# Kernel optimization log

Hardware: AMD Instinct MI355X
Metric: run time of the kernel (lower is better)

The kernel has to match this reference:

```python
import jax, jax.numpy as jnp
from jax import lax
import numpy as np

B, L, D, H, OMEGA = 8, 1024, 2048, 512, 5


def _conv1d(x_ncw, W_oiw, b):
    # x: [B, C_in, L], W: [C_out, C_in, K] -> [B, C_out, L-K+1]
    y = lax.conv_general_dilated(x_ncw, W_oiw, window_strides=(1,),
                                 padding='VALID',
                                 dimension_numbers=('NCH', 'OIH', 'NCH'))
    return y + b[None, :, None]


def _lstm_dir(xs, Wih, Whh, bih, bhh, reverse):
    # xs: [B, T, I] -> hs: [B, T, H] (PyTorch gate order i,f,g,o)
    nB, T, _ = xs.shape
    nH = Whh.shape[1]
    xs_t = jnp.swapaxes(xs, 0, 1)  # [T, B, I]
    bias = bih + bhh

    def step(carry, xt):
        h, c = carry
        g = xt @ Wih.T + h @ Whh.T + bias
        i, f, gg, o = jnp.split(g, 4, axis=-1)
        c = jax.nn.sigmoid(f) * c + jax.nn.sigmoid(i) * jnp.tanh(gg)
        h = jax.nn.sigmoid(o) * jnp.tanh(c)
        return (h, c), h

    init = (jnp.zeros((nB, nH), xs.dtype), jnp.zeros((nB, nH), xs.dtype))
    _, hs = lax.scan(step, init, xs_t, reverse=reverse)
    return jnp.swapaxes(hs, 0, 1)


def setup_inputs() -> dict:
    key = jax.random.key(0)
    ks = jax.random.split(key, 16)
    s = 0.02
    inp = {
        'x': jax.random.normal(ks[0], (B, L, D), jnp.float32),
        'Wdb': jax.random.normal(ks[1], (H, D, OMEGA), jnp.float32) * s,
        'bdb': jnp.zeros((H,), jnp.float32),
        'Wda': jax.random.normal(ks[2], (H, D, OMEGA), jnp.float32) * s,
        'bda': jnp.zeros((H,), jnp.float32),
        'Wr': jax.random.normal(ks[3], (H, D, 2 * OMEGA), jnp.float32) * s,
        'br': jnp.zeros((H,), jnp.float32),
        'Wih_fw': jax.random.normal(ks[4], (4 * H, H + 1), jnp.float32) * s,
        'Whh_fw': jax.random.normal(ks[5], (4 * H, H), jnp.float32) * s,
        'bih_fw': jnp.zeros((4 * H,), jnp.float32),
        'bhh_fw': jnp.zeros((4 * H,), jnp.float32),
        'Wih_bw': jax.random.normal(ks[6], (4 * H, H + 1), jnp.float32) * s,
        'Whh_bw': jax.random.normal(ks[7], (4 * H, H), jnp.float32) * s,
        'bih_bw': jnp.zeros((4 * H,), jnp.float32),
        'bhh_bw': jnp.zeros((4 * H,), jnp.float32),
        'Wfc': jax.random.normal(ks[8], (1, 2 * H), jnp.float32) * s,
        'bfc': jnp.zeros((1,), jnp.float32),
    }
    return inp


def reference(x, Wdb, bdb, Wda, bda, Wr, br,
              Wih_fw, Whh_fw, bih_fw, bhh_fw,
              Wih_bw, Whh_bw, bih_bw, bhh_bw, Wfc, bfc):
    T = L - 2 * OMEGA  # number of center positions
    x_c = jnp.swapaxes(x, 1, 2)  # [B, D, L]
    # Each per-window conv with kernel==window length is one output of a full
    # VALID conv; batch all centers via three full convs + offset slicing.
    db = _conv1d(x_c, Wdb, bdb)  # [B, H, L-OMEGA+1]; index t == window [t, t+OMEGA)
    da = _conv1d(x_c, Wda, bda)
    r = _conv1d(x_c, Wr, br)     # [B, H, L-2*OMEGA+1]
    # center c in [OMEGA, L-OMEGA): before window starts at c-OMEGA, after at c
    vts_d = jnp.sum(db[:, :, :T] * da[:, :, OMEGA:OMEGA + T], axis=1)  # [B, T]
    vts_r = jnp.swapaxes(r[:, :, :T], 1, 2)  # [B, T, H] (maxpool over len-1 = identity)
    joint = jnp.concatenate([vts_r, vts_d[..., None]], axis=-1)  # [B, T, H+1]
    h_fw = _lstm_dir(joint, Wih_fw, Whh_fw, bih_fw, bhh_fw, reverse=False)
    h_bw = _lstm_dir(joint, Wih_bw, Whh_bw, bih_bw, bhh_bw, reverse=True)
    lstm_out = jnp.concatenate([h_fw, h_bw], axis=-1)  # [B, T, 2H]
    logits = (lstm_out @ Wfc.T + bfc)[..., 0]  # [B, T]
    return jax.nn.sigmoid(logits)
```

## Files before the change

kernel.cpp:

```cpp
#include <hip/hip_runtime.h>

#define BB 8
#define LL 1024
#define DD 2048
#define HHH 512
#define OM 5
#define T_STEPS 1014
#define MROWS (BB * T_STEPS)
#define SENT 0xFFFFFFFFu

typedef __bf16 bf16;
typedef bf16 bf16x8 __attribute__((ext_vector_type(8)));
typedef bf16 bf16x4 __attribute__((ext_vector_type(4)));
typedef float f32x4 __attribute__((ext_vector_type(4)));
typedef unsigned int u32;
typedef unsigned long long u64;
typedef u64 u64x2 __attribute__((ext_vector_type(2)));

__device__ __forceinline__ float sigm(float x) { return 1.0f / (1.0f + __expf(-x)); }
__device__ __forceinline__ float tanh_f(float x) { return 2.0f / (1.0f + __expf(-2.0f * x)) - 1.0f; }
__device__ __forceinline__ u32 bfbits(float x) {
    bf16 b = (bf16)x;
    unsigned short s = __builtin_bit_cast(unsigned short, b);
    return (u32)s;
}
__device__ __forceinline__ float bits2f(u32 v) {
    unsigned short s = (unsigned short)(v & 0xffffu);
    return (float)__builtin_bit_cast(bf16, s);
}
__device__ __forceinline__ u64 al64(const u64* p) {
    return __hip_atomic_load(p, __ATOMIC_RELAXED, __HIP_MEMORY_SCOPE_AGENT);
}
__device__ __forceinline__ bf16x8 quad2frag(u64 lo, u64 hi) {
    u64x2 t; t[0] = lo; t[1] = hi;
    return __builtin_bit_cast(bf16x8, t);
}
__device__ __forceinline__ bool quad_ok(u64 lo, u64 hi) {
    return ((u32)lo != SENT) & ((u32)(lo >> 32) != SENT) &
           ((u32)hi != SENT) & ((u32)(hi >> 32) != SENT);
}

#if defined(__has_builtin)
#if __has_builtin(__builtin_amdgcn_global_load_lds)
#define HAS_GLL 1
#endif
#endif
#ifndef HAS_GLL
#define HAS_GLL 0
#endif

#if HAS_GLL
__device__ __forceinline__ void llds16(const bf16* g, bf16* l) {
    __builtin_amdgcn_global_load_lds((const __attribute__((address_space(1))) void*)g,
                                     (__attribute__((address_space(3))) void*)l, 16, 0, 0);
}
#endif


__global__ void cast_x_kernel(const float* __restrict__ x, bf16* __restrict__ xb, int n4) {
    int i = blockIdx.x * 256 + threadIdx.x;
    if (i >= n4) return;
    float4 v = ((const float4*)x)[i];
    bf16x4 w = { (bf16)v.x, (bf16)v.y, (bf16)v.z, (bf16)v.w };
    *(bf16x4*)(xb + (long)i * 4) = w;
}

__global__ void prep_convw(const float* __restrict__ Wdb, const float* __restrict__ Wda,
                           const float* __restrict__ Wr,
                           bf16* __restrict__ Bdb, bf16* __restrict__ Bda, bf16* __restrict__ Br) {
    int idx = blockIdx.x * 256 + threadIdx.x;
    if (idx >= HHH * DD) return;
    int h = idx >> 11, d = idx & 2047;
#pragma unroll
    for (int s = 0; s < 5; ++s) {
        Bdb[(long)h * 10240 + s * DD + d] = (bf16)Wdb[(long)(h * DD + d) * 5 + s];
        Bda[(long)h * 10240 + s * DD + d] = (bf16)Wda[(long)(h * DD + d) * 5 + s];
    }
#pragma unroll
    for (int s = 0; s < 10; ++s) {
        Br[(long)h * 20480 + s * DD + d] = (bf16)Wr[(long)(h * DD + d) * 10 + s];
    }
}

__global__ void prep_wihc(const float* __restrict__ Wih_fw, const float* __restrict__ bih_fw,
                          const float* __restrict__ bhh_fw,
                          const float* __restrict__ Wih_bw, const float* __restrict__ bih_bw,
                          const float* __restrict__ bhh_bw, bf16* __restrict__ Wihc) {
    int c = blockIdx.x;
    int tid = threadIdx.x;
    int dir = c >> 11;
    int jg = c & 2047;
    int j = jg >> 2, g = jg & 3;
    int row = g * 512 + j;
    const float* Wih = dir ? Wih_bw : Wih_fw;
    bf16* o = Wihc + (long)c * 544;
    for (int k = tid; k < 512; k += 256) o[k] = (bf16)Wih[(long)row * 513 + k];
    if (tid == 0) {
        float bias = dir ? (bih_bw[row] + bhh_bw[row]) : (bih_fw[row] + bhh_fw[row]);
        float w512 = Wih[(long)row * 513 + 512];
        bf16 hw = (bf16)w512;
        float lw = w512 - (float)hw;
        o[512] = hw; o[513] = hw; o[514] = (bf16)lw; o[515] = (bf16)bias;
    }
    if (tid >= 4 && tid < 32) o[512 + tid] = (bf16)0.0f;
}

__global__ void init_kernel(u32* __restrict__ hf, u32* __restrict__ hb) {
    const long n4 = (long)(T_STEPS + 1) * 1024;
    long i = (long)blockIdx.x * 256 + threadIdx.x;
    if (i >= 2 * n4) return;
    u32* base = (i < n4) ? hf : hb;
    long k = (i < n4) ? i : (i - n4);
    u32 v = (k < 1024) ? 0u : SENT;
    uint4 val; val.x = v; val.y = v; val.z = v; val.w = v;
    ((uint4*)base)[k] = val;
}

__global__ __launch_bounds__(256, 2)
void gemm_bt(const bf16* __restrict__ A, const bf16* __restrict__ Bm, void* __restrict__ Cout,
             const float* __restrict__ cbias, int M, int K, int windowed, int shift,
             int lda, int ldc, int cmode) {
    __shared__ bf16 Ash[128 * 32];
    __shared__ bf16 Bsh[128 * 32];
    const int tid = threadIdx.x;
    const int m0 = blockIdx.x * 128;
    const int n0 = blockIdx.y * 128;

    long aoff[2], boff[2];
#pragma unroll
    for (int it = 0; it < 2; ++it) {
        int idx = it * 256 + tid;
        int r = idx & 127, koct = idx >> 7;
        int mg = m0 + r; if (mg >= M) mg = M - 1;
        long abase;
        if (windowed) {
            int b = mg / T_STEPS;
            int t = mg - b * T_STEPS;
            abase = ((long)(b * LL + t + shift)) * DD;
        } else {
            abase = (long)mg * lda;
        }
        aoff[it] = abase + koct * 8;
        boff[it] = (long)(n0 + r) * K + koct * 8;
    }

    const int wave = tid >> 6, lane = tid & 63;
    const int wr = (wave >> 1) * 64;
    const int wc = (wave & 1) * 64;
    const int q = lane >> 4, mm = lane & 15;

    f32x4 acc[4][4] = {};

    for (int k0 = 0; k0 < K; k0 += 32) {
#if HAS_GLL
        __syncthreads();
#pragma unroll
        for (int it = 0; it < 2; ++it) {
            bf16* la = Ash + (size_t)(it * 256 + wave * 64) * 8;
            bf16* lb = Bsh + (size_t)(it * 256 + wave * 64) * 8;
            llds16(A + aoff[it] + k0, la);
            llds16(Bm + boff[it] + k0, lb);
        }
        __syncthreads();
#else
        uint4 av[2], bv[2];
#pragma unroll
        for (int it = 0; it < 2; ++it) {
            av[it] = *(const uint4*)(A + aoff[it] + k0);
            bv[it] = *(const uint4*)(Bm + boff[it] + k0);
        }
        __syncthreads();
#pragma unroll
        for (int it = 0; it < 2; ++it) {
            int idx = it * 256 + tid;
            *(uint4*)((char*)Ash + idx * 16) = av[it];
            *(uint4*)((char*)Bsh + idx * 16) = bv[it];
        }
        __syncthreads();
#endif
        bf16x8 af[4], bfr[4];
#pragma unroll
        for (int i = 0; i < 4; ++i) {
            af[i]  = *(const bf16x8*)((char*)Ash + q * 2048 + (wr + i * 16 + mm) * 16);
            bfr[i] = *(const bf16x8*)((char*)Bsh + q * 2048 + (wc + i * 16 + mm) * 16);
        }
#pragma unroll
        for (int i = 0; i < 4; ++i)
#pragma unroll
            for (int j = 0; j < 4; ++j)
                acc[i][j] = __builtin_amdgcn_mfma_f32_16x16x32_bf16(af[i], bfr[j], acc[i][j], 0, 0, 0);
    }

#pragma unroll
    for (int i = 0; i < 4; ++i) {
        int rowb = m0 + wr + i * 16 + q * 4;
#pragma unroll
        for (int j = 0; j < 4; ++j) {
            int col = n0 + wc + j * 16 + mm;
            float bias = cbias ? cbias[col] : 0.0f;
#pragma unroll
            for (int r = 0; r < 4; ++r) {
                int gr = rowb + r;
                if (gr < M) {
                    float v = acc[i][j][r] + bias;
                    if (cmode == 0) ((float*)Cout)[(long)gr * ldc + col] = v;
                    else            ((bf16*)Cout)[(long)gr * ldc + col] = (bf16)v;
                }
            }
        }
    }
}

__global__ void vts_kernel(const float* __restrict__ dbuf, const float* __restrict__ dabuf,
                           bf16* __restrict__ joint) {
    int gid = blockIdx.x * blockDim.x + threadIdx.x;
    int wid = gid >> 6, lane = gid & 63;
    if (wid >= MROWS) return;
    const float* p1 = dbuf + (long)wid * 512 + lane * 8;
    const float* p2 = dabuf + (long)wid * 512 + lane * 8;
    float s = 0.0f;
#pragma unroll
    for (int j = 0; j < 8; ++j) s += p1[j] * p2[j];
#pragma unroll
    for (int off = 32; off > 0; off >>= 1) s += __shfl_down(s, off);
    bf16* row = joint + (long)wid * 544;
    if (lane == 0) {
        bf16 hv = (bf16)s;
        float lo = s - (float)hv;
        row[512] = hv; row[513] = (bf16)lo; row[514] = hv; row[515] = (bf16)1.0f;
    }
    if (lane >= 4 && lane < 32) row[512 + lane] = (bf16)0.0f;
}

__global__ __launch_bounds__(64) __attribute__((amdgpu_waves_per_eu(1, 1)))
void lstm_kernel(const float* __restrict__ Whh_fw, const float* __restrict__ Whh_bw,
                 const float* __restrict__ gih, u32* __restrict__ hist_fw,
                 u32* __restrict__ hist_bw) {
    const int wgid = blockIdx.x;
    const int dir = wgid >> 6;
    const int w = wgid & 63;
    const int j0 = w * 8;
    const int lane = threadIdx.x;
    const float* Whh = dir ? Whh_bw : Whh_fw;
    u32* hist = dir ? hist_bw : hist_fw;

    const int q = lane >> 4, mm = lane & 15;

    bf16x8 afrag[2][16];
#pragma unroll
    for (int mt = 0; mt < 2; ++mt) {
        int rl = mt * 16 + mm;
        int u = rl >> 2, g = rl & 3;
        const float* wrow = Whh + ((long)(g * 512 + j0 + u)) * 512;
#pragma unroll
        for (int ks = 0; ks < 16; ++ks) {
            int base = ks * 32 + q * 8;
            bf16x8 f;
#pragma unroll
            for (int j = 0; j < 8; ++j) {
                int col = base + (j >> 1) + ((j & 1) << 2);
                f[j] = (bf16)wrow[col];
            }
            afrag[mt][ks] = f;
        }
    }

    float c0 = 0.0f, c1 = 0.0f;
    const bool valid = (mm < 8);
    const int bcl = valid ? mm : 0;

    int tcur = dir ? (T_STEPS - 1) : 0;
    const float* gp0 = gih + ((long)(bcl * T_STEPS + tcur)) * 4096 + dir * 2048 + (j0 + q) * 4;
    f32x4 pg0 = *(const f32x4*)gp0;
    f32x4 pg1 = *(const f32x4*)(gp0 + 16);

    for (int s = 0; s < T_STEPS; ++s) {
        const u64* hrow = (const u64*)(hist + (long)s * 4096 + mm * 256);
        u64 wa[16], wb[16];
#pragma unroll
        for (int i = 0; i < 16; ++i) { wa[i] = 0ull; wb[i] = 0ull; }

        u32 pa = valid ? 0xFFu : 0u;
        if (valid) {
#pragma unroll
            for (int ks = 0; ks < 8; ++ks) {
                const u64* p = hrow + ks * 8 + q * 2;
                wa[2 * ks]     = al64(p + 0);
                wa[2 * ks + 1] = al64(p + 1);
            }
        }
        for (;;) {
#pragma unroll
            for (int ks = 0; ks < 8; ++ks) {
                if (pa & (1u << ks)) {
                    if (quad_ok(wa[2 * ks], wa[2 * ks + 1])) pa &= ~(1u << ks);
                }
            }
            if (__all((int)(pa == 0u))) break;
            __builtin_amdgcn_s_sleep(1);
#pragma unroll
            for (int ks = 0; ks < 8; ++ks) {
                if (pa & (1u << ks)) {
                    const u64* p = hrow + ks * 8 + q * 2;
                    wa[2 * ks]     = al64(p + 0);
                    wa[2 * ks + 1] = al64(p + 1);
                }
            }
        }

        u32 pb = valid ? 0xFFu : 0u;
        if (valid) {
#pragma unroll
            for (int ks = 0; ks < 8; ++ks) {
                const u64* p = hrow + (ks + 8) * 8 + q * 2;
                wb[2 * ks]     = al64(p + 0);
                wb[2 * ks + 1] = al64(p + 1);
            }
        }

        f32x4 acc0 = pg0, acc1 = pg1;
        f32x4 acc0b = {0.0f, 0.0f, 0.0f, 0.0f}, acc1b = {0.0f, 0.0f, 0.0f, 0.0f};

        if (s + 1 < T_STEPS) {
            int tn = dir ? (T_STEPS - 2 - s) : (s + 1);
            const float* gpn = gih + ((long)(bcl * T_STEPS + tn)) * 4096 + dir * 2048 + (j0 + q) * 4;
            pg0 = *(const f32x4*)gpn;
            pg1 = *(const f32x4*)(gpn + 16);
        }

#pragma unroll
        for (int ks = 0; ks < 8; ++ks) {
            bf16x8 b = quad2frag(wa[2 * ks], wa[2 * ks + 1]);
            acc0 = __builtin_amdgcn_mfma_f32_16x16x32_bf16(afrag[0][ks], b, acc0, 0, 0, 0);
            acc1 = __builtin_amdgcn_mfma_f32_16x16x32_bf16(afrag[1][ks], b, acc1, 0, 0, 0);
        }

        for (;;) {
#pragma unroll
            for (int ks = 0; ks < 8; ++ks) {
                if (pb & (1u << ks)) {
                    if (quad_ok(wb[2 * ks], wb[2 * ks + 1])) pb &= ~(1u << ks);
                }
            }
            if (__all((int)(pb == 0u))) break;
            __builtin_amdgcn_s_sleep(1);
#pragma unroll
            for (int ks = 0; ks < 8; ++ks) {
                if (pb & (1u << ks)) {
                    const u64* p = hrow + (ks + 8) * 8 + q * 2;
                    wb[2 * ks]     = al64(p + 0);
                    wb[2 * ks + 1] = al64(p + 1);
                }
            }
        }

#pragma unroll
        for (int ks = 0; ks < 8; ++ks) {
            bf16x8 b = quad2frag(wb[2 * ks], wb[2 * ks + 1]);
            acc0b = __builtin_amdgcn_mfma_f32_16x16x32_bf16(afrag[0][ks + 8], b, acc0b, 0, 0, 0);
            acc1b = __builtin_amdgcn_mfma_f32_16x16x32_bf16(afrag[1][ks + 8], b, acc1b, 0, 0, 0);
        }
        acc0 += acc0b;
        acc1 += acc1b;

        float ig = sigm(acc0[0]), fg = sigm(acc0[1]), gg = tanh_f(acc0[2]), og = sigm(acc0[3]);
        c0 = fg * c0 + ig * gg;
        float h0 = og * tanh_f(c0);
        ig = sigm(acc1[0]); fg = sigm(acc1[1]); gg = tanh_f(acc1[2]); og = sigm(acc1[3]);
        c1 = fg * c1 + ig * gg;
        float h1 = og * tanh_f(c1);

        if (valid) {
            u32 pw = bfbits(h0) | (bfbits(h1) << 16);
            __hip_atomic_store(hist + (long)(s + 1) * 4096 + mm * 256 + (j0 >> 1) + q, pw,
                               __ATOMIC_RELAXED, __HIP_MEMORY_SCOPE_AGENT);
        }
    }
}

__global__ void final_fc(const u32* __restrict__ hist_fw, const u32* __restrict__ hist_bw,
                         const float* __restrict__ Wfc, const float* __restrict__ bfc,
                         float* __restrict__ out) {
    int gid = blockIdx.x * blockDim.x + threadIdx.x;
    int wid = gid >> 6, lane = gid & 63;
    if (wid >= MROWS) return;
    int b = wid / T_STEPS, t = wid - b * T_STEPS;
    const u32* hf = hist_fw + (long)(t + 1) * 4096 + b * 256 + lane * 4;
    const u32* hb = hist_bw + (long)(T_STEPS - t) * 4096 + b * 256 + lane * 4;
    float s = 0.0f;
#pragma unroll
    for (int i = 0; i < 4; ++i) {
        u32 wf = hf[i], wb = hb[i];
        s += bits2f(wf) * Wfc[8 * lane + i] + bits2f(wf >> 16) * Wfc[8 * lane + 4 + i];
        s += bits2f(wb) * Wfc[512 + 8 * lane + i] + bits2f(wb >> 16) * Wfc[512 + 8 * lane + 4 + i];
    }
#pragma unroll
    for (int off = 32; off > 0; off >>= 1) s += __shfl_down(s, off);
    if (lane == 0) out[wid] = 1.0f / (1.0f + __expf(-(s + bfc[0])));
}


extern "C" void kernel_launch(void* const* d_in, const int* in_sizes, int n_in,
                              void* d_out, int out_size, void* d_ws, size_t ws_size,
                              hipStream_t stream) {
    const float* x      = (const float*)d_in[0];
    const float* Wdb    = (const float*)d_in[1];
    const float* bdb    = (const float*)d_in[2];
    const float* Wda    = (const float*)d_in[3];
    const float* bda    = (const float*)d_in[4];
    const float* Wr     = (const float*)d_in[5];
    const float* br     = (const float*)d_in[6];
    const float* Wih_fw = (const float*)d_in[7];
    const float* Whh_fw = (const float*)d_in[8];
    const float* bih_fw = (const float*)d_in[9];
    const float* bhh_fw = (const float*)d_in[10];
    const float* Wih_bw = (const float*)d_in[11];
    const float* Whh_bw = (const float*)d_in[12];
    const float* bih_bw = (const float*)d_in[13];
    const float* bhh_bw = (const float*)d_in[14];
    const float* Wfc    = (const float*)d_in[15];
    const float* bfc    = (const float*)d_in[16];
    float* out = (float*)d_out;

    char* p = (char*)d_ws;
    auto alloc = [&](size_t bytes) { char* r = p; p += (bytes + 255) & ~(size_t)255; return r; };
    bf16* Wihc    = (bf16*)alloc((size_t)4096 * 544 * 2);
    bf16* joint   = (bf16*)alloc((size_t)MROWS * 544 * 2);
    u32* hist_fw  = (u32*)alloc((size_t)(T_STEPS + 1) * 4096 * 4);
    u32* hist_bw  = (u32*)alloc((size_t)(T_STEPS + 1) * 4096 * 4);
    char* q0 = p;
    bf16* xb      = (bf16*)alloc((size_t)BB * LL * DD * 2);
    bf16* Bdb     = (bf16*)alloc((size_t)512 * 10240 * 2);
    bf16* Bda     = (bf16*)alloc((size_t)512 * 10240 * 2);
    bf16* Br      = (bf16*)alloc((size_t)512 * 20480 * 2);
    float* dbuf   = (float*)alloc((size_t)MROWS * 512 * 4);
    float* dabuf  = (float*)alloc((size_t)MROWS * 512 * 4);
    float* gih    = (float*)q0;
    (void)ws_size;

    cast_x_kernel<<<16384, 256, 0, stream>>>(x, xb, BB * LL * DD / 4);
    prep_convw<<<4096, 256, 0, stream>>>(Wdb, Wda, Wr, Bdb, Bda, Br);
    prep_wihc<<<4096, 256, 0, stream>>>(Wih_fw, bih_fw, bhh_fw, Wih_bw, bih_bw, bhh_bw, Wihc);
    {
        long n4 = (long)(T_STEPS + 1) * 1024 * 2;
        init_kernel<<<(int)((n4 + 255) / 256), 256, 0, stream>>>(hist_fw, hist_bw);
    }

    dim3 g1(64, 4);
    gemm_bt<<<g1, 256, 0, stream>>>(xb, Bdb, dbuf, bdb, MROWS, 10240, 1, 0, 0, 512, 0);
    gemm_bt<<<g1, 256, 0, stream>>>(xb, Bda, dabuf, bda, MROWS, 10240, 1, 5, 0, 512, 0);
    gemm_bt<<<g1, 256, 0, stream>>>(xb, Br, joint, br, MROWS, 20480, 1, 0, 0, 544, 1);
    vts_kernel<<<(MROWS * 64 + 255) / 256, 256, 0, stream>>>(dbuf, dabuf, joint);

    dim3 g2(64, 32);
    gemm_bt<<<g2, 256, 0, stream>>>(joint, Wihc, gih, nullptr, MROWS, 544, 0, 0, 544, 4096, 0);

    lstm_kernel<<<dim3(128), dim3(64), 0, stream>>>(Whh_fw, Whh_bw, gih, hist_fw, hist_bw);

    final_fc<<<(MROWS * 64 + 255) / 256, 256, 0, stream>>>(hist_fw, hist_bw, Wfc, bfc, out);
}
```

Measured before the change: 5.136 ms.

## Interleave forward and backward LSTM directions in one workgroup to overlap sync latency

New measurement: 8.882 ms. 1.73x slower.

```diff
diff --git a/kernel.cpp b/kernel.cpp
--- a/kernel.cpp
+++ b/kernel.cpp
@@ -236,144 +236,185 @@
 void lstm_kernel(const float* __restrict__ Whh_fw, const float* __restrict__ Whh_bw,
                  const float* __restrict__ gih, u32* __restrict__ hist_fw,
                  u32* __restrict__ hist_bw) {
-    const int wgid = blockIdx.x;
-    const int dir = wgid >> 6;
-    const int w = wgid & 63;
+    const int w = blockIdx.x;
     const int j0 = w * 8;
     const int lane = threadIdx.x;
-    const float* Whh = dir ? Whh_bw : Whh_fw;
-    u32* hist = dir ? hist_bw : hist_fw;
-
     const int q = lane >> 4, mm = lane & 15;
-
-    bf16x8 afrag[2][16];
+    const bool valid = (mm < 8);
+    const int bcl = valid ? mm : 0;
+
+    bf16x8 afF[2][16], afB[2][16];
 #pragma unroll
     for (int mt = 0; mt < 2; ++mt) {
         int rl = mt * 16 + mm;
         int u = rl >> 2, g = rl & 3;
-        const float* wrow = Whh + ((long)(g * 512 + j0 + u)) * 512;
+        const float* wrF = Whh_fw + ((long)(g * 512 + j0 + u)) * 512;
+        const float* wrB = Whh_bw + ((long)(g * 512 + j0 + u)) * 512;
 #pragma unroll
         for (int ks = 0; ks < 16; ++ks) {
             int base = ks * 32 + q * 8;
-            bf16x8 f;
+            bf16x8 fF, fB;
 #pragma unroll
             for (int j = 0; j < 8; ++j) {
                 int col = base + (j >> 1) + ((j & 1) << 2);
-                f[j] = (bf16)wrow[col];
-            }
-            afrag[mt][ks] = f;
-        }
-    }
-
-    float c0 = 0.0f, c1 = 0.0f;
-    const bool valid = (mm < 8);
-    const int bcl = valid ? mm : 0;
-
-    int tcur = dir ? (T_STEPS - 1) : 0;
-    const float* gp0 = gih + ((long)(bcl * T_STEPS + tcur)) * 4096 + dir * 2048 + (j0 + q) * 4;
-    f32x4 pg0 = *(const f32x4*)gp0;
-    f32x4 pg1 = *(const f32x4*)(gp0 + 16);
+                fF[j] = (bf16)wrF[col];
+                fB[j] = (bf16)wrB[col];
+            }
+            afF[mt][ks] = fF;
+            afB[mt][ks] = fB;
+        }
+    }
+
+    float cF0 = 0.0f, cF1 = 0.0f, cB0 = 0.0f, cB1 = 0.0f;
+
+    const float* gF0p = gih + ((long)(bcl * T_STEPS + 0)) * 4096 + (j0 + q) * 4;
+    const float* gB0p = gih + ((long)(bcl * T_STEPS + (T_STEPS - 1))) * 4096 + 2048 + (j0 + q) * 4;
+    f32x4 pgF0 = *(const f32x4*)gF0p, pgF1 = *(const f32x4*)(gF0p + 16);
+    f32x4 pgB0 = *(const f32x4*)gB0p, pgB1 = *(const f32x4*)(gB0p + 16);
+
+    u64 wvF[32], wvB[32];
+#pragma unroll
+    for (int i = 0; i < 32; ++i) { wvF[i] = 0ull; wvB[i] = 0ull; }
+    u32 pF = 0u, pB = 0u;
+
+    if (valid) {
+        const u64* hqF = (const u64*)(hist_fw + 0 + mm * 256);
+        const u64* hqB = (const u64*)(hist_bw + 0 + mm * 256);
+#pragma unroll
+        for (int ks = 0; ks < 16; ++ks) {
+            const u64* ppF = hqF + ks * 8 + q * 2;
+            const u64* ppB = hqB + ks * 8 + q * 2;
+            wvF[2 * ks] = al64(ppF + 0); wvF[2 * ks + 1] = al64(ppF + 1);
+            wvB[2 * ks] = al64(ppB + 0); wvB[2 * ks + 1] = al64(ppB + 1);
+        }
+        pF = 0xFFFFu; pB = 0xFFFFu;
+    }
 
     for (int s = 0; s < T_STEPS; ++s) {
-        const u64* hrow = (const u64*)(hist + (long)s * 4096 + mm * 256);
-        u64 wa[16], wb[16];
-#pragma unroll
-        for (int i = 0; i < 16; ++i) { wa[i] = 0ull; wb[i] = 0ull; }
-
-        u32 pa = valid ? 0xFFu : 0u;
-        if (valid) {
+        {
+            const u64* hq = (const u64*)(hist_fw + (long)s * 4096 + mm * 256);
+            for (;;) {
+#pragma unroll
+                for (int ks = 0; ks < 16; ++ks)
+                    if (pF & (1u << ks))
+                        if (quad_ok(wvF[2 * ks], wvF[2 * ks + 1])) pF &= ~(1u << ks);
+                if (__all((int)(pF == 0u))) break;
+                __builtin_amdgcn_s_sleep(1);
+#pragma unroll
+                for (int ks = 0; ks < 16; ++ks)
+                    if (pF & (1u << ks)) {
+                        const u64* pp = hq + ks * 8 + q * 2;
+                        wvF[2 * ks]     = al64(pp + 0);
+                        wvF[2 * ks + 1] = al64(pp + 1);
+                    }
+            }
+
+            f32x4 a0 = pgF0, a1 = pgF1;
+            f32x4 b0 = {0.0f, 0.0f, 0.0f, 0.0f}, b1 = {0.0f, 0.0f, 0.0f, 0.0f};
+
+            if (s + 1 < T_STEPS) {
+                const float* gpn = gih + ((long)(bcl * T_STEPS + (s + 1))) * 4096 + (j0 + q) * 4;
+                pgF0 = *(const f32x4*)gpn;
+                pgF1 = *(const f32x4*)(gpn + 16);
+            }
+
 #pragma unroll
             for (int ks = 0; ks < 8; ++ks) {
-                const u64* p = hrow + ks * 8 + q * 2;
-                wa[2 * ks]     = al64(p + 0);
-                wa[2 * ks + 1] = al64(p + 1);
-            }
-        }
-        for (;;) {
+                bf16x8 blo = quad2frag(wvF[2 * ks], wvF[2 * ks + 1]);
+                bf16x8 bhi = quad2frag(wvF[2 * (ks + 8)], wvF[2 * (ks + 8) + 1]);
+                a0 = __builtin_amdgcn_mfma_f32_16x16x32_bf16(afF[0][ks], blo, a0, 0, 0, 0);
+                a1 = __builtin_amdgcn_mfma_f32_16x16x32_bf16(afF[1][ks], blo, a1, 0, 0, 0);
+                b0 = __builtin_amdgcn_mfma_f32_16x16x32_bf16(afF[0][ks + 8], bhi, b0, 0, 0, 0);
+                b1 = __builtin_amdgcn_mfma_f32_16x16x32_bf16(afF[1][ks + 8], bhi, b1, 0, 0, 0);
+            }
+            a0 += b0; a1 += b1;
+
+            float ig = sigm(a0[0]), fg = sigm(a0[1]), gg = tanh_f(a0[2]), og = sigm(a0[3]);
+            cF0 = fg * cF0 + ig * gg;
+            float h0 = og * tanh_f(cF0);
+            ig = sigm(a1[0]); fg = sigm(a1[1]); gg = tanh_f(a1[2]); og = sigm(a1[3]);
+            cF1 = fg * cF1 + ig * gg;
+            float h1 = og * tanh_f(cF1);
+
+            if (valid) {
+                u32 pw = bfbits(h0) | (bfbits(h1) << 16);
+                __hip_atomic_store(hist_fw + (long)(s + 1) * 4096 + mm * 256 + (j0 >> 1) + q, pw,
+                                   __ATOMIC_RELAXED, __HIP_MEMORY_SCOPE_AGENT);
+            }
+
+            if (s + 1 < T_STEPS && valid) {
+                const u64* hqn = (const u64*)(hist_fw + (long)(s + 1) * 4096 + mm * 256);
+#pragma unroll
+                for (int ks = 0; ks < 16; ++ks) {
+                    const u64* pp = hqn + ks * 8 + q * 2;
+                    wvF[2 * ks]     = al64(pp + 0);
+                    wvF[2 * ks + 1] = al64(pp + 1);
+                }
+                pF = 0xFFFFu;
+            }
+        }
+
+        {
+            const u64* hq = (const u64*)(hist_bw + (long)s * 4096 + mm * 256);
+            for (;;) {
+#pragma unroll
+                for (int ks = 0; ks < 16; ++ks)
+                    if (pB & (1u << ks))
+                        if (quad_ok(wvB[2 * ks], wvB[2 * ks + 1])) pB &= ~(1u << ks);
+                if (__all((int)(pB == 0u))) break;
+                __builtin_amdgcn_s_sleep(1);
+#pragma unroll
+                for (int ks = 0; ks < 16; ++ks)
+                    if (pB & (1u << ks)) {
+                        const u64* pp = hq + ks * 8 + q * 2;
+                        wvB[2 * ks]     = al64(pp + 0);
+                        wvB[2 * ks + 1] = al64(pp + 1);
+                    }
+            }
+
+            f32x4 a0 = pgB0, a1 = pgB1;
+            f32x4 b0 = {0.0f, 0.0f, 0.0f, 0.0f}, b1 = {0.0f, 0.0f, 0.0f, 0.0f};
+
+            if (s + 1 < T_STEPS) {
+                const float* gpn = gih + ((long)(bcl * T_STEPS + (T_STEPS - 2 - s))) * 4096 + 2048 + (j0 + q) * 4;
+                pgB0 = *(const f32x4*)gpn;
+                pgB1 = *(const f32x4*)(gpn + 16);
+            }
+
 #pragma unroll
             for (int ks = 0; ks < 8; ++ks) {
-                if (pa & (1u << ks)) {
-                    if (quad_ok(wa[2 * ks], wa[2 * ks + 1])) pa &= ~(1u << ks);
+                bf16x8 blo = quad2frag(wvB[2 * ks], wvB[2 * ks + 1]);
+                bf16x8 bhi = quad2frag(wvB[2 * (ks + 8)], wvB[2 * (ks + 8) + 1]);
+                a0 = __builtin_amdgcn_mfma_f32_16x16x32_bf16(afB[0][ks], blo, a0, 0, 0, 0);
+                a1 = __builtin_amdgcn_mfma_f32_16x16x32_bf16(afB[1][ks], blo, a1, 0, 0, 0);
+                b0 = __builtin_amdgcn_mfma_f32_16x16x32_bf16(afB[0][ks + 8], bhi, b0, 0, 0, 0);
+                b1 = __builtin_amdgcn_mfma_f32_16x16x32_bf16(afB[1][ks + 8], bhi, b1, 0, 0, 0);
+            }
+            a0 += b0; a1 += b1;
+
+            float ig = sigm(a0[0]), fg = sigm(a0[1]), gg = tanh_f(a0[2]), og = sigm(a0[3]);
+            cB0 = fg * cB0 + ig * gg;
+            float h0 = og * tanh_f(cB0);
+            ig = sigm(a1[0]); fg = sigm(a1[1]); gg = tanh_f(a1[2]); og = sigm(a1[3]);
+            cB1 = fg * cB1 + ig * gg;
+            float h1 = og * tanh_f(cB1);
+
+            if (valid) {
+                u32 pw = bfbits(h0) | (bfbits(h1) << 16);
+                __hip_atomic_store(hist_bw + (long)(s + 1) * 4096 + mm * 256 + (j0 >> 1) + q, pw,
+                                   __ATOMIC_RELAXED, __HIP_MEMORY_SCOPE_AGENT);
+            }
+
+            if (s + 1 < T_STEPS && valid) {
+                const u64* hqn = (const u64*)(hist_bw + (long)(s + 1) * 4096 + mm * 256);
+#pragma unroll
+                for (int ks = 0; ks < 16; ++ks) {
+                    const u64* pp = hqn + ks * 8 + q * 2;
+                    wvB[2 * ks]     = al64(pp + 0);
+                    wvB[2 * ks + 1] = al64(pp + 1);
                 }
-            }
-            if (__all((int)(pa == 0u))) break;
-            __builtin_amdgcn_s_sleep(1);
-#pragma unroll
-            for (int ks = 0; ks < 8; ++ks) {
-                if (pa & (1u << ks)) {
-                    const u64* p = hrow + ks * 8 + q * 2;
-                    wa[2 * ks]     = al64(p + 0);
-                    wa[2 * ks + 1] = al64(p + 1);
-                }
-            }
-        }
-
-        u32 pb = valid ? 0xFFu : 0u;
-        if (valid) {
-#pragma unroll
-            for (int ks = 0; ks < 8; ++ks) {
-                const u64* p = hrow + (ks + 8) * 8 + q * 2;
-                wb[2 * ks]     = al64(p + 0);
-                wb[2 * ks + 1] = al64(p + 1);
-            }
-        }
-
-        f32x4 acc0 = pg0, acc1 = pg1;
-        f32x4 acc0b = {0.0f, 0.0f, 0.0f, 0.0f}, acc1b = {0.0f, 0.0f, 0.0f, 0.0f};
-
-        if (s + 1 < T_STEPS) {
-            int tn = dir ? (T_STEPS - 2 - s) : (s + 1);
-            const float* gpn = gih + ((long)(bcl * T_STEPS + tn)) * 4096 + dir * 2048 + (j0 + q) * 4;
-            pg0 = *(const f32x4*)gpn;
-            pg1 = *(const f32x4*)(gpn + 16);
-        }
-
-#pragma unroll
-        for (int ks = 0; ks < 8; ++ks) {
-            bf16x8 b = quad2frag(wa[2 * ks], wa[2 * ks + 1]);
-            acc0 = __builtin_amdgcn_mfma_f32_16x16x32_bf16(afrag[0][ks], b, acc0, 0, 0, 0);
-            acc1 = __builtin_amdgcn_mfma_f32_16x16x32_bf16(afrag[1][ks], b, acc1, 0, 0, 0);
-        }
-
-        for (;;) {
-#pragma unroll
-            for (int ks = 0; ks < 8; ++ks) {
-                if (pb & (1u << ks)) {
-                    if (quad_ok(wb[2 * ks], wb[2 * ks + 1])) pb &= ~(1u << ks);
-                }
-            }
-            if (__all((int)(pb == 0u))) break;
-            __builtin_amdgcn_s_sleep(1);
-#pragma unroll
-            for (int ks = 0; ks < 8; ++ks) {
-                if (pb & (1u << ks)) {
-                    const u64* p = hrow + (ks + 8) * 8 + q * 2;
-                    wb[2 * ks]     = al64(p + 0);
-                    wb[2 * ks + 1] = al64(p + 1);
-                }
-            }
-        }
-
-#pragma unroll
-        for (int ks = 0; ks < 8; ++ks) {
-            bf16x8 b = quad2frag(wb[2 * ks], wb[2 * ks + 1]);
-            acc0b = __builtin_amdgcn_mfma_f32_16x16x32_bf16(afrag[0][ks + 8], b, acc0b, 0, 0, 0);
-            acc1b = __builtin_amdgcn_mfma_f32_16x16x32_bf16(afrag[1][ks + 8], b, acc1b, 0, 0, 0);
-        }
-        acc0 += acc0b;
-        acc1 += acc1b;
-
-        float ig = sigm(acc0[0]), fg = sigm(acc0[1]), gg = tanh_f(acc0[2]), og = sigm(acc0[3]);
-        c0 = fg * c0 + ig * gg;
-        float h0 = og * tanh_f(c0);
-        ig = sigm(acc1[0]); fg = sigm(acc1[1]); gg = tanh_f(acc1[2]); og = sigm(acc1[3]);
-        c1 = fg * c1 + ig * gg;
-        float h1 = og * tanh_f(c1);
-
-        if (valid) {
-            u32 pw = bfbits(h0) | (bfbits(h1) << 16);
-            __hip_atomic_store(hist + (long)(s + 1) * 4096 + mm * 256 + (j0 >> 1) + q, pw,
-                               __ATOMIC_RELAXED, __HIP_MEMORY_SCOPE_AGENT);
+                pB = 0xFFFFu;
+            }
         }
     }
 }
@@ -455,7 +496,7 @@
     dim3 g2(64, 32);
     gemm_bt<<<g2, 256, 0, stream>>>(joint, Wihc, gih, nullptr, MROWS, 544, 0, 0, 544, 4096, 0);
 
-    lstm_kernel<<<dim3(128), dim3(64), 0, stream>>>(Whh_fw, Whh_bw, gih, hist_fw, hist_bw);
+    lstm_kernel<<<dim3(64), dim3(64), 0, stream>>>(Whh_fw, Whh_bw, gih, hist_fw, hist_bw);
 
     final_fc<<<(MROWS * 64 + 255) / 256, 256, 0, stream>>>(hist_fw, hist_bw, Wfc, bfc, out);
 }
```
